# Optimization experiments

Measured on AMD Instinct MI355X. Metric: run time of the kernel, lower is better.

The kernel has to match this reference:

```python
import jax, jax.numpy as jnp
import numpy as np

D_MODEL = 1024
N_HEADS = 16
D_K = D_MODEL // N_HEADS
D_FF = 4096
EPS = 1e-5


def layer_norm(x, gamma, beta):
    mu = jnp.mean(x, axis=-1, keepdims=True)
    var = jnp.var(x, axis=-1, keepdims=True)
    return (x - mu) * jax.lax.rsqrt(var + EPS) * gamma + beta


def setup_inputs() -> dict:
    key = jax.random.key(0)
    ks = jax.random.split(key, 16)
    B, S = 4, 1024
    s = 0.02
    inp = {
        "x": jax.random.normal(ks[0], (B, S, D_MODEL), dtype=jnp.float32),
        "mask": jnp.ones((B, 1, 1, S), dtype=jnp.int32),
        "Wq": jax.random.normal(ks[1], (D_MODEL, D_MODEL), jnp.float32) * s,
        "bq": jnp.zeros((D_MODEL,), jnp.float32),
        "Wk": jax.random.normal(ks[2], (D_MODEL, D_MODEL), jnp.float32) * s,
        "bk": jnp.zeros((D_MODEL,), jnp.float32),
        "Wv": jax.random.normal(ks[3], (D_MODEL, D_MODEL), jnp.float32) * s,
        "bv": jnp.zeros((D_MODEL,), jnp.float32),
        "Wo": jax.random.normal(ks[4], (D_MODEL, D_MODEL), jnp.float32) * s,
        "bo": jnp.zeros((D_MODEL,), jnp.float32),
        "W1": jax.random.normal(ks[5], (D_MODEL, D_FF), jnp.float32) * s,
        "b1": jnp.zeros((D_FF,), jnp.float32),
        "W2": jax.random.normal(ks[6], (D_FF, D_MODEL), jnp.float32) * s,
        "b2": jnp.zeros((D_MODEL,), jnp.float32),
        "ln1_g": jnp.ones((D_MODEL,), jnp.float32),
        "ln1_b": jnp.zeros((D_MODEL,), jnp.float32),
        "ln2_g": jnp.ones((D_MODEL,), jnp.float32),
        "ln2_b": jnp.zeros((D_MODEL,), jnp.float32),
    }
    return inp


def reference(x, mask, Wq, bq, Wk, bk, Wv, bv, Wo, bo, W1, b1, W2, b2,
              ln1_g, ln1_b, ln2_g, ln2_b):
    B, S, _ = x.shape
    # QKV projections -> [B, H, S, d_k]
    def split_heads(t):
        return t.reshape(B, S, N_HEADS, D_K).transpose(0, 2, 1, 3)
    Q = split_heads(x @ Wq + bq)
    K = split_heads(x @ Wk + bk)
    V = split_heads(x @ Wv + bv)
    # scores [B, H, S, S]
    scores = jnp.einsum('bhqd,bhkd->bhqk', Q, K) / jnp.sqrt(jnp.float32(D_K))
    scores = jnp.where(mask == 0, jnp.float32(-1e9), scores)
    attn = jax.nn.softmax(scores, axis=-1)
    ctx = jnp.einsum('bhqk,bhkd->bhqd', attn, V)
    ctx = ctx.transpose(0, 2, 1, 3).reshape(B, S, D_MODEL)
    attn_out = ctx @ Wo + bo
    # residual + LN (dropout is identity in eval)
    h = layer_norm(x + attn_out, ln1_g, ln1_b)
    ff = jax.nn.relu(h @ W1 + b1) @ W2 + b2
    return layer_norm(h + ff, ln2_g, ln2_b)
```

## Files before the change

### kernel.cpp

```cpp
#include <hip/hip_runtime.h>
#include <hip/hip_bf16.h>

typedef __attribute__((ext_vector_type(8))) short bf16x8;
typedef __attribute__((ext_vector_type(4))) short bf16x4;
typedef __attribute__((ext_vector_type(4))) float f32x4;
typedef unsigned int u32;
typedef unsigned short ush;

#define SEQ 1024
#define MTOT 4096

__device__ __forceinline__ ush f2bf(float f){
  u32 u = __float_as_uint(f);
  u32 r = (u + 0x7fffu + ((u >> 16) & 1u)) >> 16;
  return (ush)r;
}

__device__ __forceinline__ f32x4 mfma16(bf16x8 a, bf16x8 b, f32x4 c){
  return __builtin_amdgcn_mfma_f32_16x16x32_bf16(a, b, c, 0, 0, 0);
}

__device__ __forceinline__ void gload_lds16(const ush* g, ush* l){
  __builtin_amdgcn_global_load_lds(
      (const __attribute__((address_space(1))) u32*)g,
      (__attribute__((address_space(3))) u32*)l, 16, 0, 0);
}

__global__ __launch_bounds__(256) void cvt_kernel(const float* __restrict__ src,
                                                  ush* __restrict__ dst, int n){
  int i = (blockIdx.x * 256 + threadIdx.x) * 4;
  if (i < n){
    float4 v = *(const float4*)&src[i];
    ushort4 o = { f2bf(v.x), f2bf(v.y), f2bf(v.z), f2bf(v.w) };
    *(ushort4*)&dst[i] = o;
  }
}

__global__ __launch_bounds__(256) void tconv_kernel(const float* __restrict__ src,
                                                    ush* __restrict__ dst, int R, int C){
  __shared__ float t[32][33];
  int tx = threadIdx.x & 31, ty = threadIdx.x >> 5;
  int r0 = blockIdx.y * 32, c0 = blockIdx.x * 32;
  #pragma unroll
  for (int i = 0; i < 32; i += 8)
    t[ty + i][tx] = src[(size_t)(r0 + ty + i) * C + (c0 + tx)];
  __syncthreads();
  #pragma unroll
  for (int i = 0; i < 32; i += 8)
    dst[(size_t)(c0 + ty + i) * R + (r0 + tx)] = f2bf(t[tx][ty + i]);
}

__global__ __launch_bounds__(256) void biaspack_kernel(const float* __restrict__ bq,
    const float* __restrict__ bk, const float* __restrict__ bv, float* __restrict__ dst){
  int i = blockIdx.x * 256 + threadIdx.x;
  if (i < 3072){
    float v = (i < 1024) ? bq[i] : (i < 2048) ? bk[i - 1024] : bv[i - 2048];
    dst[i] = v;
  }
}

__device__ __forceinline__ void stage_piece(ush* piece, const ush* g0, int K,
                                            int tid, int w){
  #pragma unroll
  for (int I = 0; I < 2; I++){
    int c = I * 512 + tid;
    int r = c >> 2;
    int gl = (c & 3) ^ ((r >> 1) & 3);
    gload_lds16(g0 + (size_t)r * K + gl * 8, piece + I * 4096 + w * 512);
  }
}

__device__ __forceinline__ bf16x8 frag(const ush* piece, int row, int g){
  int phys = g ^ ((row >> 1) & 3);
  return *(const bf16x8*)(piece + row * 32 + phys * 8);
}

#define PH_BAR_TOP() do{ __builtin_amdgcn_sched_barrier(0); \
  __builtin_amdgcn_s_barrier(); \
  asm volatile("s_waitcnt lgkmcnt(0)" ::: "memory"); \
  __builtin_amdgcn_sched_barrier(0); \
  __builtin_amdgcn_s_setprio(1); }while(0)
#define PH_BAR_BOT() do{ __builtin_amdgcn_s_setprio(0); \
  __builtin_amdgcn_sched_barrier(0); \
  __builtin_amdgcn_s_barrier(); }while(0)

template<int RELU, int OUTF32>
__global__ __launch_bounds__(512, 2) void gemm8_kernel(
    const ush* __restrict__ A, const ush* __restrict__ Bt,
    const float* __restrict__ bias,
    ush* __restrict__ Cb, float* __restrict__ Cf,
    int M, int N, int K, int ldc, int ksl)
{
  __shared__ ush lds[2][2][2][8192];
  const int tid = threadIdx.x;
  const int lane = tid & 63, w = tid >> 6;
  const int g = lane >> 4, qr = lane & 15;
  const int wr = w >> 2, wc = w & 3;
  const int gx = gridDim.x;
  const int nwg = gx * gridDim.y;
  const int id = blockIdx.y * gx + blockIdx.x;
  const int swz = (id & 7) * (nwg >> 3) + (id >> 3);
  const int bn = (swz % gx) * 256;
  const int bm = (swz / gx) * 256;
  const int kbase = blockIdx.z * ksl;
  const int NT = ksl >> 6;
  const ush* Ab = A  + (size_t)bm * K + kbase;
  const ush* Bb = Bt + (size_t)bn * K + kbase;

  stage_piece(lds[0][0][0], Ab,      K, tid, w);
  stage_piece(lds[0][1][0], Bb,      K, tid, w);
  stage_piece(lds[0][0][1], Ab + 32, K, tid, w);
  stage_piece(lds[0][1][1], Bb + 32, K, tid, w);
  if (NT > 1){
    stage_piece(lds[1][0][0], Ab + 64, K, tid, w);
    stage_piece(lds[1][1][0], Bb + 64, K, tid, w);
  }
  asm volatile("s_waitcnt vmcnt(4)" ::: "memory");
  __builtin_amdgcn_sched_barrier(0);
  __builtin_amdgcn_s_barrier();

  f32x4 acc[8][4] = {};
  const int ar = wr * 128 + qr;
  const int br = wc * 64 + qr;

  for (int T = 0; T < NT; ++T){
    const int cb = T & 1, nb = cb ^ 1;
    const ush* An = Ab + (size_t)(T + 1) * 64;
    const ush* Bn = Bb + (size_t)(T + 1) * 64;
    const ush* Af = Ab + (size_t)(T + 2) * 64;
    const ush* Bf = Bb + (size_t)(T + 2) * 64;
    bf16x8 af[4], bfr[4];

    #pragma unroll
    for (int j = 0; j < 4; j++) bfr[j] = frag(lds[cb][1][0], br + j * 16, g);
    #pragma unroll
    for (int i = 0; i < 4; i++) af[i] = frag(lds[cb][0][0], ar + i * 16, g);
    if (T + 1 < NT) stage_piece(lds[nb][0][1], An + 32, K, tid, w);
    PH_BAR_TOP();
    #pragma unroll
    for (int i = 0; i < 4; i++)
      #pragma unroll
      for (int j = 0; j < 4; j++)
        acc[i][j] = mfma16(af[i], bfr[j], acc[i][j]);
    PH_BAR_BOT();

    #pragma unroll
    for (int i = 0; i < 4; i++) af[i] = frag(lds[cb][0][0], ar + 64 + i * 16, g);
    if (T + 1 < NT) stage_piece(lds[nb][1][1], Bn + 32, K, tid, w);
    PH_BAR_TOP();
    #pragma unroll
    for (int i = 0; i < 4; i++)
      #pragma unroll
      for (int j = 0; j < 4; j++)
        acc[4 + i][j] = mfma16(af[i], bfr[j], acc[4 + i][j]);
    PH_BAR_BOT();

    #pragma unroll
    for (int j = 0; j < 4; j++) bfr[j] = frag(lds[cb][1][1], br + j * 16, g);
    #pragma unroll
    for (int i = 0; i < 4; i++) af[i] = frag(lds[cb][0][1], ar + i * 16, g);
    if (T + 2 < NT) stage_piece(lds[cb][0][0], Af, K, tid, w);
    PH_BAR_TOP();
    #pragma unroll
    for (int i = 0; i < 4; i++)
      #pragma unroll
      for (int j = 0; j < 4; j++)
        acc[i][j] = mfma16(af[i], bfr[j], acc[i][j]);
    PH_BAR_BOT();

    #pragma unroll
    for (int i = 0; i < 4; i++) af[i] = frag(lds[cb][0][1], ar + 64 + i * 16, g);
    if (T + 2 < NT) stage_piece(lds[cb][1][0], Bf, K, tid, w);
    PH_BAR_TOP();
    #pragma unroll
    for (int i = 0; i < 4; i++)
      #pragma unroll
      for (int j = 0; j < 4; j++)
        acc[4 + i][j] = mfma16(af[i], bfr[j], acc[4 + i][j]);
    __builtin_amdgcn_s_setprio(0);
    __builtin_amdgcn_sched_barrier(0);
    asm volatile("s_waitcnt vmcnt(4)" ::: "memory");
    __builtin_amdgcn_sched_barrier(0);
    __builtin_amdgcn_s_barrier();
  }

  float* Cfz = Cf;
  if (OUTF32) Cfz = Cf + (size_t)blockIdx.z * M * ldc;
  #pragma unroll
  for (int j = 0; j < 4; j++){
    const int col = bn + wc * 64 + j * 16 + qr;
    const float bv = OUTF32 ? 0.f : bias[col];
    #pragma unroll
    for (int i = 0; i < 8; i++){
      const int row0 = bm + wr * 128 + i * 16 + g * 4;
      #pragma unroll
      for (int rr = 0; rr < 4; rr++){
        float v = acc[i][j][rr] + bv;
        if (RELU) v = fmaxf(v, 0.f);
        const size_t idx = (size_t)(row0 + rr) * ldc + col;
        if (OUTF32) Cfz[idx] = v; else Cb[idx] = f2bf(v);
      }
    }
  }
}

__global__ __launch_bounds__(256) void attn_kernel(
    const ush* __restrict__ qkv, const int* __restrict__ mask,
    ush* __restrict__ ctx)
{
  __shared__ ush Vt[64 * 40];
  __shared__ ush Pl[4][16 * 40];
  __shared__ int mk[1024];
  const int tid = threadIdx.x;
  const int lane = tid & 63, w = tid >> 6;
  const int g = lane >> 4, qr = lane & 15;
  const int hb = blockIdx.y;
  const int b = hb >> 4, hh = hb & 15;
  const int qt = blockIdx.x;

  { int4 mv = *(const int4*)&mask[b * SEQ + tid * 4]; *(int4*)&mk[tid * 4] = mv; }
  __syncthreads();

  const size_t rowQ = (size_t)(b * SEQ + qt * 64 + w * 16 + qr);
  const ush* Qp = qkv + rowQ * 3072 + hh * 64;
  bf16x8 qf0 = *(const bf16x8*)(Qp + g * 8);
  bf16x8 qf1 = *(const bf16x8*)(Qp + 32 + g * 8);

  const ush* Kb = qkv + (size_t)b * SEQ * 3072 + 1024 + hh * 64;
  const ush* Vb = qkv + (size_t)b * SEQ * 3072 + 2048 + hh * 64;

  f32x4 oa[4] = {};
  float m_run = -1e30f, l_run = 0.f;
  const int vkey = tid >> 3, vd0 = (tid & 7) * 8;

  for (int kt = 0; kt < SEQ / 32; ++kt){
    const int k0 = kt * 32;
    bf16x8 vv = *(const bf16x8*)(Vb + (size_t)(k0 + vkey) * 3072 + vd0);
    const ush* Kr0 = Kb + (size_t)(k0 + qr) * 3072;
    const ush* Kr1 = Kr0 + (size_t)16 * 3072;
    bf16x8 ka0 = *(const bf16x8*)(Kr0 + g * 8);
    bf16x8 ka1 = *(const bf16x8*)(Kr0 + 32 + g * 8);
    bf16x8 kb0 = *(const bf16x8*)(Kr1 + g * 8);
    bf16x8 kb1 = *(const bf16x8*)(Kr1 + 32 + g * 8);
    f32x4 z = {0.f, 0.f, 0.f, 0.f};
    f32x4 st0 = mfma16(ka0, qf0, z); st0 = mfma16(ka1, qf1, st0);
    f32x4 st1 = mfma16(kb0, qf0, z); st1 = mfma16(kb1, qf1, st1);
    float sc[8];
    #pragma unroll
    for (int r = 0; r < 4; r++){
      int key = k0 + g * 4 + r;
      sc[r]     = (mk[key] == 0)      ? -1e9f : st0[r] * 0.125f;
      sc[4 + r] = (mk[key + 16] == 0) ? -1e9f : st1[r] * 0.125f;
    }
    float pm = sc[0];
    #pragma unroll
    for (int r = 1; r < 8; r++) pm = fmaxf(pm, sc[r]);
    pm = fmaxf(pm, __shfl_xor(pm, 16));
    pm = fmaxf(pm, __shfl_xor(pm, 32));
    float m_new = fmaxf(m_run, pm);
    float corr = __expf(m_run - m_new);
    float ls = 0.f;
    #pragma unroll
    for (int r = 0; r < 8; r++){ sc[r] = __expf(sc[r] - m_new); ls += sc[r]; }
    ls += __shfl_xor(ls, 16); ls += __shfl_xor(ls, 32);
    l_run = l_run * corr + ls; m_run = m_new;
    #pragma unroll
    for (int r = 0; r < 4; r++){
      float cr = __shfl(corr, g * 4 + r);
      oa[0][r] *= cr; oa[1][r] *= cr; oa[2][r] *= cr; oa[3][r] *= cr;
    }
    bf16x4 p0, p1;
    #pragma unroll
    for (int r = 0; r < 4; r++){ p0[r] = (short)f2bf(sc[r]); p1[r] = (short)f2bf(sc[4 + r]); }
    *(bf16x4*)&Pl[w][qr * 40 + g * 4]      = p0;
    *(bf16x4*)&Pl[w][qr * 40 + 16 + g * 4] = p1;
    __syncthreads();
    #pragma unroll
    for (int j = 0; j < 8; j++) Vt[(vd0 + j) * 40 + vkey] = (ush)vv[j];
    __syncthreads();
    bf16x8 pf = *(const bf16x8*)&Pl[w][qr * 40 + g * 8];
    #pragma unroll
    for (int d = 0; d < 4; d++){
      bf16x8 vf = *(const bf16x8*)&Vt[(d * 16 + qr) * 40 + g * 8];
      oa[d] = mfma16(pf, vf, oa[d]);
    }
  }
  float linv = 1.f / l_run;
  #pragma unroll
  for (int r = 0; r < 4; r++){
    float lr = __shfl(linv, g * 4 + r);
    size_t rowO = (size_t)(b * SEQ + qt * 64 + w * 16 + g * 4 + r);
    #pragma unroll
    for (int d = 0; d < 4; d++)
      ctx[rowO * 1024 + hh * 64 + d * 16 + qr] = f2bf(oa[d][r] * lr);
  }
}

template<bool WB>
__global__ __launch_bounds__(256) void ln4_kernel(
    const float* __restrict__ X, const float* __restrict__ P,
    const float* __restrict__ bias,
    const float* __restrict__ gam, const float* __restrict__ bet,
    float* __restrict__ Of, ush* __restrict__ Ob)
{
  const int row = blockIdx.x, tid = threadIdx.x;
  const size_t base = (size_t)row * 1024 + tid * 4;
  float4 xv = *(const float4*)&X[base];
  float4 bv4 = *(const float4*)&bias[tid * 4];
  float s0 = xv.x + bv4.x, s1 = xv.y + bv4.y, s2 = xv.z + bv4.z, s3 = xv.w + bv4.w;
  #pragma unroll
  for (int z = 0; z < 4; z++){
    float4 p = *(const float4*)&P[(size_t)z * 4194304 + base];
    s0 += p.x; s1 += p.y; s2 += p.z; s3 += p.w;
  }
  float sum = s0 + s1 + s2 + s3;
  float sq  = s0 * s0 + s1 * s1 + s2 * s2 + s3 * s3;
  #pragma unroll
  for (int o = 1; o < 64; o <<= 1){ sum += __shfl_xor(sum, o); sq += __shfl_xor(sq, o); }
  __shared__ float red[8];
  int lane = tid & 63, w = tid >> 6;
  if (lane == 0){ red[w] = sum; red[4 + w] = sq; }
  __syncthreads();
  sum = red[0] + red[1] + red[2] + red[3];
  sq  = red[4] + red[5] + red[6] + red[7];
  float mean = sum * (1.f / 1024.f);
  float var  = sq * (1.f / 1024.f) - mean * mean;
  float rs = rsqrtf(var + 1e-5f);
  float4 gv = *(const float4*)&gam[tid * 4];
  float4 bt = *(const float4*)&bet[tid * 4];
  float o0 = (s0 - mean) * rs * gv.x + bt.x;
  float o1 = (s1 - mean) * rs * gv.y + bt.y;
  float o2 = (s2 - mean) * rs * gv.z + bt.z;
  float o3 = (s3 - mean) * rs * gv.w + bt.w;
  float4 ov = { o0, o1, o2, o3 };
  *(float4*)&Of[base] = ov;
  if (WB){
    ushort4 ob = { f2bf(o0), f2bf(o1), f2bf(o2), f2bf(o3) };
    *(ushort4*)&Ob[base] = ob;
  }
}

extern "C" void kernel_launch(void* const* d_in, const int* in_sizes, int n_in,
                              void* d_out, int out_size, void* d_ws, size_t ws_size,
                              hipStream_t stream)
{
  const float* x    = (const float*)d_in[0];
  const int*   mask = (const int*)  d_in[1];
  const float* Wq = (const float*)d_in[2];
  const float* bq = (const float*)d_in[3];
  const float* Wk = (const float*)d_in[4];
  const float* bk = (const float*)d_in[5];
  const float* Wv = (const float*)d_in[6];
  const float* bv = (const float*)d_in[7];
  const float* Wo = (const float*)d_in[8];
  const float* bo = (const float*)d_in[9];
  const float* W1 = (const float*)d_in[10];
  const float* b1 = (const float*)d_in[11];
  const float* W2 = (const float*)d_in[12];
  const float* b2 = (const float*)d_in[13];
  const float* g1 = (const float*)d_in[14];
  const float* be1= (const float*)d_in[15];
  const float* g2 = (const float*)d_in[16];
  const float* be2= (const float*)d_in[17];
  float* out = (float*)d_out;

  char* ws = (char*)d_ws;
  size_t off = 0;
  auto alloc = [&](size_t bytes)->void*{ void* p = ws + off; off += (bytes + 255) & ~(size_t)255; return p; };
  ush* xb     = (ush*)alloc((size_t)MTOT * 1024 * 2);
  ush* wqkvT  = (ush*)alloc((size_t)3072 * 1024 * 2);
  ush* woT    = (ush*)alloc((size_t)1024 * 1024 * 2);
  ush* w1T    = (ush*)alloc((size_t)4096 * 1024 * 2);
  ush* w2T    = (ush*)alloc((size_t)1024 * 4096 * 2);
  float* bqkv = (float*)alloc(3072 * 4);
  ush* qkv    = (ush*)alloc((size_t)MTOT * 3072 * 2);
  ush* ctx    = (ush*)alloc((size_t)MTOT * 1024 * 2);
  float* part = (float*)alloc((size_t)4 * MTOT * 1024 * 4);
  float* h    = (float*)alloc((size_t)MTOT * 1024 * 4);
  ush* hb     = (ush*)alloc((size_t)MTOT * 1024 * 2);
  ush* ff1    = qkv;

  cvt_kernel<<<dim3(4096), dim3(256), 0, stream>>>(x, xb, MTOT * 1024);
  tconv_kernel<<<dim3(32, 32), dim3(256), 0, stream>>>(Wq, wqkvT,               1024, 1024);
  tconv_kernel<<<dim3(32, 32), dim3(256), 0, stream>>>(Wk, wqkvT + 1024 * 1024, 1024, 1024);
  tconv_kernel<<<dim3(32, 32), dim3(256), 0, stream>>>(Wv, wqkvT + 2048 * 1024, 1024, 1024);
  tconv_kernel<<<dim3(32, 32), dim3(256), 0, stream>>>(Wo, woT,                 1024, 1024);
  tconv_kernel<<<dim3(128, 32), dim3(256), 0, stream>>>(W1, w1T, 1024, 4096);
  tconv_kernel<<<dim3(32, 128), dim3(256), 0, stream>>>(W2, w2T, 4096, 1024);
  biaspack_kernel<<<dim3(12), dim3(256), 0, stream>>>(bq, bk, bv, bqkv);

  gemm8_kernel<0, 0><<<dim3(12, 16, 1), dim3(512), 0, stream>>>(
      xb, wqkvT, bqkv, qkv, nullptr, MTOT, 3072, 1024, 3072, 1024);

  attn_kernel<<<dim3(16, 64), dim3(256), 0, stream>>>(qkv, mask, ctx);

  gemm8_kernel<0, 1><<<dim3(4, 16, 4), dim3(512), 0, stream>>>(
      ctx, woT, nullptr, nullptr, part, MTOT, 1024, 1024, 1024, 256);

  ln4_kernel<true><<<dim3(4096), dim3(256), 0, stream>>>(x, part, bo, g1, be1, h, hb);

  gemm8_kernel<1, 0><<<dim3(16, 16, 1), dim3(512), 0, stream>>>(
      hb, w1T, b1, ff1, nullptr, MTOT, 4096, 1024, 4096, 1024);

  gemm8_kernel<0, 1><<<dim3(4, 16, 4), dim3(512), 0, stream>>>(
      ff1, w2T, nullptr, nullptr, part, MTOT, 1024, 4096, 1024, 1024);

  ln4_kernel<false><<<dim3(4096), dim3(256), 0, stream>>>(h, part, b2, g2, be2, out, nullptr);
}
```

Before: 416.6 us.

## Rewrite attention with 32x32 MFMA, pretransposed V, exp2 softmax and lazy rescale

Replaces the flash-attention kernel with a version using 32x32x16 bf16 MFMA tiles, 32 queries per wave and 64-key blocks. V is pretransposed by a new kernel so it can be read directly as MFMA operands, and P is packed in registers with cvt_pk and permlane32 swaps rather than staged through LDS with block barriers. The QKV GEMM epilogue folds the 1/sqrt(dk)*log2e scale into Q so softmax can use exp2. The running max is only rescaled when it grows by more than 8, and per-key masking is skipped when the whole mask row is ones. The cost is an extra transpose kernel, extra workspace, and a bit of precision loss from the delayed rescale.

```diff
diff --git a/kernel.cpp b/kernel.cpp
--- a/kernel.cpp
+++ b/kernel.cpp
@@ -2,13 +2,20 @@
 #include <hip/hip_bf16.h>
 
 typedef __attribute__((ext_vector_type(8))) short bf16x8;
-typedef __attribute__((ext_vector_type(4))) short bf16x4;
 typedef __attribute__((ext_vector_type(4))) float f32x4;
+typedef __attribute__((ext_vector_type(16))) float f32x16;
 typedef unsigned int u32;
 typedef unsigned short ush;
 
 #define SEQ 1024
 #define MTOT 4096
+#define QSCALE_LOG2 0.18033688f
+
+#if __has_builtin(__builtin_amdgcn_exp2f)
+#define EXP2(x) __builtin_amdgcn_exp2f(x)
+#else
+#define EXP2(x) exp2f(x)
+#endif
 
 __device__ __forceinline__ ush f2bf(float f){
   u32 u = __float_as_uint(f);
@@ -18,6 +25,13 @@
 
 __device__ __forceinline__ f32x4 mfma16(bf16x8 a, bf16x8 b, f32x4 c){
   return __builtin_amdgcn_mfma_f32_16x16x32_bf16(a, b, c, 0, 0, 0);
+}
+__device__ __forceinline__ f32x16 mfma32(bf16x8 a, bf16x8 b, f32x16 c){
+  return __builtin_amdgcn_mfma_f32_32x32x16_bf16(a, b, c, 0, 0, 0);
+}
+
+__device__ __forceinline__ u32 cvtpk(float lo, float hi){
+  u32 r; asm("v_cvt_pk_bf16_f32 %0, %1, %2" : "=v"(r) : "v"(lo), "v"(hi)); return r;
 }
 
 __device__ __forceinline__ void gload_lds16(const ush* g, ush* l){
@@ -57,6 +71,21 @@
     float v = (i < 1024) ? bq[i] : (i < 2048) ? bk[i - 1024] : bv[i - 2048];
     dst[i] = v;
   }
+}
+
+__global__ __launch_bounds__(256) void vtrans_kernel(const ush* __restrict__ qkv,
+                                                     ush* __restrict__ VT){
+  __shared__ ush t[32][34];
+  int tx = threadIdx.x & 31, ty = threadIdx.x >> 5;
+  int bh = blockIdx.z, b = bh >> 4, h = bh & 15;
+  int k0 = blockIdx.x * 32, d0 = blockIdx.y * 32;
+  #pragma unroll
+  for (int i = 0; i < 32; i += 8)
+    t[ty + i][tx] = qkv[(size_t)(b * SEQ + k0 + ty + i) * 3072 + 2048 + h * 64 + d0 + tx];
+  __syncthreads();
+  #pragma unroll
+  for (int i = 0; i < 32; i += 8)
+    VT[(size_t)(bh * 64 + d0 + ty + i) * SEQ + k0 + tx] = t[tx][ty + i];
 }
 
 __device__ __forceinline__ void stage_piece(ush* piece, const ush* g0, int K,
@@ -84,7 +113,7 @@
   __builtin_amdgcn_sched_barrier(0); \
   __builtin_amdgcn_s_barrier(); }while(0)
 
-template<int RELU, int OUTF32>
+template<int RELU, int OUTF32, int SCALEQ>
 __global__ __launch_bounds__(512, 2) void gemm8_kernel(
     const ush* __restrict__ A, const ush* __restrict__ Bt,
     const float* __restrict__ bias,
@@ -190,6 +219,7 @@
   for (int j = 0; j < 4; j++){
     const int col = bn + wc * 64 + j * 16 + qr;
     const float bv = OUTF32 ? 0.f : bias[col];
+    const float scl = (SCALEQ && col < 1024) ? QSCALE_LOG2 : 1.f;
     #pragma unroll
     for (int i = 0; i < 8; i++){
       const int row0 = bm + wr * 128 + i * 16 + g * 4;
@@ -197,6 +227,7 @@
       for (int rr = 0; rr < 4; rr++){
         float v = acc[i][j][rr] + bv;
         if (RELU) v = fmaxf(v, 0.f);
+        if (SCALEQ) v *= scl;
         const size_t idx = (size_t)(row0 + rr) * ldc + col;
         if (OUTF32) Cfz[idx] = v; else Cb[idx] = f2bf(v);
       }
@@ -204,95 +235,131 @@
   }
 }
 
-__global__ __launch_bounds__(256) void attn_kernel(
-    const ush* __restrict__ qkv, const int* __restrict__ mask,
-    ush* __restrict__ ctx)
+__global__ __launch_bounds__(256) void attn2_kernel(
+    const ush* __restrict__ qkv, const ush* __restrict__ VT,
+    const int* __restrict__ mask, ush* __restrict__ ctx)
 {
-  __shared__ ush Vt[64 * 40];
-  __shared__ ush Pl[4][16 * 40];
-  __shared__ int mk[1024];
   const int tid = threadIdx.x;
   const int lane = tid & 63, w = tid >> 6;
-  const int g = lane >> 4, qr = lane & 15;
-  const int hb = blockIdx.y;
-  const int b = hb >> 4, hh = hb & 15;
-  const int qt = blockIdx.x;
-
-  { int4 mv = *(const int4*)&mask[b * SEQ + tid * 4]; *(int4*)&mk[tid * 4] = mv; }
+  const int c = lane & 31, hi = lane >> 5;
+  const int bh = blockIdx.y, b = bh >> 4, hh = bh & 15;
+  const int q0 = blockIdx.x * 128 + w * 32;
+
+  __shared__ int mflag;
+  if (tid == 0) mflag = 1;
   __syncthreads();
-
-  const size_t rowQ = (size_t)(b * SEQ + qt * 64 + w * 16 + qr);
-  const ush* Qp = qkv + rowQ * 3072 + hh * 64;
-  bf16x8 qf0 = *(const bf16x8*)(Qp + g * 8);
-  bf16x8 qf1 = *(const bf16x8*)(Qp + 32 + g * 8);
-
-  const ush* Kb = qkv + (size_t)b * SEQ * 3072 + 1024 + hh * 64;
-  const ush* Vb = qkv + (size_t)b * SEQ * 3072 + 2048 + hh * 64;
-
-  f32x4 oa[4] = {};
+  {
+    int4 mv = *(const int4*)&mask[b * SEQ + tid * 4];
+    if (!(mv.x && mv.y && mv.z && mv.w)) mflag = 0;
+  }
+  __syncthreads();
+  const bool maskall = (mflag != 0);
+
+  const ush* Qrow = qkv + (size_t)(b * SEQ + q0 + c) * 3072 + hh * 64;
+  bf16x8 qf[4];
+  #pragma unroll
+  for (int kd = 0; kd < 4; kd++)
+    qf[kd] = *(const bf16x8*)(Qrow + kd * 16 + hi * 8);
+
+  const ush* Kb  = qkv + (size_t)(b * SEQ) * 3072 + 1024 + hh * 64;
+  const ush* VTb = VT + (size_t)(bh * 64) * SEQ;
+
+  f32x16 o0 = {}, o1 = {};
   float m_run = -1e30f, l_run = 0.f;
-  const int vkey = tid >> 3, vd0 = (tid & 7) * 8;
-
-  for (int kt = 0; kt < SEQ / 32; ++kt){
-    const int k0 = kt * 32;
-    bf16x8 vv = *(const bf16x8*)(Vb + (size_t)(k0 + vkey) * 3072 + vd0);
-    const ush* Kr0 = Kb + (size_t)(k0 + qr) * 3072;
-    const ush* Kr1 = Kr0 + (size_t)16 * 3072;
-    bf16x8 ka0 = *(const bf16x8*)(Kr0 + g * 8);
-    bf16x8 ka1 = *(const bf16x8*)(Kr0 + 32 + g * 8);
-    bf16x8 kb0 = *(const bf16x8*)(Kr1 + g * 8);
-    bf16x8 kb1 = *(const bf16x8*)(Kr1 + 32 + g * 8);
-    f32x4 z = {0.f, 0.f, 0.f, 0.f};
-    f32x4 st0 = mfma16(ka0, qf0, z); st0 = mfma16(ka1, qf1, st0);
-    f32x4 st1 = mfma16(kb0, qf0, z); st1 = mfma16(kb1, qf1, st1);
-    float sc[8];
-    #pragma unroll
-    for (int r = 0; r < 4; r++){
-      int key = k0 + g * 4 + r;
-      sc[r]     = (mk[key] == 0)      ? -1e9f : st0[r] * 0.125f;
-      sc[4 + r] = (mk[key + 16] == 0) ? -1e9f : st1[r] * 0.125f;
-    }
-    float pm = sc[0];
-    #pragma unroll
-    for (int r = 1; r < 8; r++) pm = fmaxf(pm, sc[r]);
-    pm = fmaxf(pm, __shfl_xor(pm, 16));
-    pm = fmaxf(pm, __shfl_xor(pm, 32));
-    float m_new = fmaxf(m_run, pm);
-    float corr = __expf(m_run - m_new);
+
+  bf16x8 kf[8];
+  #pragma unroll
+  for (int kb = 0; kb < 2; kb++)
+    #pragma unroll
+    for (int kd = 0; kd < 4; kd++)
+      kf[kb * 4 + kd] = *(const bf16x8*)(Kb + (size_t)(kb * 32 + c) * 3072 + kd * 16 + hi * 8);
+
+  for (int t = 0; t < SEQ / 64; ++t){
+    const int k0 = t * 64;
+    bf16x8 vf[8];
+    #pragma unroll
+    for (int db = 0; db < 2; db++)
+      #pragma unroll
+      for (int ks = 0; ks < 4; ks++)
+        vf[db * 4 + ks] = *(const bf16x8*)(VTb + (size_t)(db * 32 + c) * SEQ + k0 + ks * 16 + hi * 8);
+
+    f32x16 s0 = {}, s1 = {};
+    #pragma unroll
+    for (int kd = 0; kd < 4; kd++){
+      s0 = mfma32(kf[kd],     qf[kd], s0);
+      s1 = mfma32(kf[4 + kd], qf[kd], s1);
+    }
+
+    float p[32];
+    #pragma unroll
+    for (int r = 0; r < 16; r++){ p[r] = s0[r]; p[16 + r] = s1[r]; }
+
+    if (!maskall){
+      #pragma unroll
+      for (int r32 = 0; r32 < 32; r32++){
+        int r = r32 & 15;
+        int key = (r32 >> 4) * 32 + (r & 3) + 8 * (r >> 2) + 4 * hi;
+        if (mask[b * SEQ + k0 + key] == 0) p[r32] = -1e9f;
+      }
+    }
+
+    if (t + 1 < SEQ / 64){
+      #pragma unroll
+      for (int kb = 0; kb < 2; kb++)
+        #pragma unroll
+        for (int kd = 0; kd < 4; kd++)
+          kf[kb * 4 + kd] = *(const bf16x8*)(Kb + (size_t)(k0 + 64 + kb * 32 + c) * 3072 + kd * 16 + hi * 8);
+    }
+
+    float pmax = p[0];
+    #pragma unroll
+    for (int r = 1; r < 32; r++) pmax = fmaxf(pmax, p[r]);
+    pmax = fmaxf(pmax, __shfl_xor(pmax, 32));
+    if (__any(pmax > m_run + 8.f)){
+      float m_new = fmaxf(m_run, pmax);
+      float corr = EXP2(m_run - m_new);
+      l_run *= corr;
+      m_run = m_new;
+      #pragma unroll
+      for (int r = 0; r < 16; r++){
+        float cr = __shfl(corr, (r & 3) + 8 * (r >> 2) + 4 * hi);
+        o0[r] *= cr; o1[r] *= cr;
+      }
+    }
     float ls = 0.f;
     #pragma unroll
-    for (int r = 0; r < 8; r++){ sc[r] = __expf(sc[r] - m_new); ls += sc[r]; }
-    ls += __shfl_xor(ls, 16); ls += __shfl_xor(ls, 32);
-    l_run = l_run * corr + ls; m_run = m_new;
-    #pragma unroll
-    for (int r = 0; r < 4; r++){
-      float cr = __shfl(corr, g * 4 + r);
-      oa[0][r] *= cr; oa[1][r] *= cr; oa[2][r] *= cr; oa[3][r] *= cr;
-    }
-    bf16x4 p0, p1;
-    #pragma unroll
-    for (int r = 0; r < 4; r++){ p0[r] = (short)f2bf(sc[r]); p1[r] = (short)f2bf(sc[4 + r]); }
-    *(bf16x4*)&Pl[w][qr * 40 + g * 4]      = p0;
-    *(bf16x4*)&Pl[w][qr * 40 + 16 + g * 4] = p1;
-    __syncthreads();
-    #pragma unroll
-    for (int j = 0; j < 8; j++) Vt[(vd0 + j) * 40 + vkey] = (ush)vv[j];
-    __syncthreads();
-    bf16x8 pf = *(const bf16x8*)&Pl[w][qr * 40 + g * 8];
-    #pragma unroll
-    for (int d = 0; d < 4; d++){
-      bf16x8 vf = *(const bf16x8*)&Vt[(d * 16 + qr) * 40 + g * 8];
-      oa[d] = mfma16(pf, vf, oa[d]);
-    }
-  }
+    for (int r = 0; r < 32; r++){ p[r] = EXP2(p[r] - m_run); ls += p[r]; }
+    ls += __shfl_xor(ls, 32);
+    l_run += ls;
+
+    union { u32 wdw[4]; bf16x8 v; } af[4];
+    #pragma unroll
+    for (int ks = 0; ks < 4; ks++){
+      int b0 = (ks >> 1) * 16 + 8 * (ks & 1);
+      u32 c00 = cvtpk(p[b0],     p[b0 + 1]);
+      u32 c01 = cvtpk(p[b0 + 2], p[b0 + 3]);
+      u32 c10 = cvtpk(p[b0 + 4], p[b0 + 5]);
+      u32 c11 = cvtpk(p[b0 + 6], p[b0 + 7]);
+      asm volatile("v_permlane32_swap_b32 %0, %1" : "+v"(c10), "+v"(c00));
+      asm volatile("v_permlane32_swap_b32 %0, %1" : "+v"(c11), "+v"(c01));
+      af[ks].wdw[0] = c00; af[ks].wdw[1] = c01; af[ks].wdw[2] = c10; af[ks].wdw[3] = c11;
+    }
+
+    #pragma unroll
+    for (int ks = 0; ks < 4; ks++){
+      o0 = mfma32(af[ks].v, vf[ks],     o0);
+      o1 = mfma32(af[ks].v, vf[4 + ks], o1);
+    }
+  }
+
   float linv = 1.f / l_run;
   #pragma unroll
-  for (int r = 0; r < 4; r++){
-    float lr = __shfl(linv, g * 4 + r);
-    size_t rowO = (size_t)(b * SEQ + qt * 64 + w * 16 + g * 4 + r);
-    #pragma unroll
-    for (int d = 0; d < 4; d++)
-      ctx[rowO * 1024 + hh * 64 + d * 16 + qr] = f2bf(oa[d][r] * lr);
+  for (int r = 0; r < 16; r++){
+    int crow = (r & 3) + 8 * (r >> 2) + 4 * hi;
+    float li = __shfl(linv, crow);
+    size_t base = (size_t)(b * SEQ + q0 + crow) * 1024 + hh * 64;
+    ctx[base + c]      = f2bf(o0[r] * li);
+    ctx[base + 32 + c] = f2bf(o1[r] * li);
   }
 }
 
@@ -378,6 +445,7 @@
   float* part = (float*)alloc((size_t)4 * MTOT * 1024 * 4);
   float* h    = (float*)alloc((size_t)MTOT * 1024 * 4);
   ush* hb     = (ush*)alloc((size_t)MTOT * 1024 * 2);
+  ush* VT     = (ush*)alloc((size_t)64 * 64 * SEQ * 2);
   ush* ff1    = qkv;
 
   cvt_kernel<<<dim3(4096), dim3(256), 0, stream>>>(x, xb, MTOT * 1024);
@@ -389,20 +457,22 @@
   tconv_kernel<<<dim3(32, 128), dim3(256), 0, stream>>>(W2, w2T, 4096, 1024);
   biaspack_kernel<<<dim3(12), dim3(256), 0, stream>>>(bq, bk, bv, bqkv);
 
-  gemm8_kernel<0, 0><<<dim3(12, 16, 1), dim3(512), 0, stream>>>(
+  gemm8_kernel<0, 0, 1><<<dim3(12, 16, 1), dim3(512), 0, stream>>>(
       xb, wqkvT, bqkv, qkv, nullptr, MTOT, 3072, 1024, 3072, 1024);
 
-  attn_kernel<<<dim3(16, 64), dim3(256), 0, stream>>>(qkv, mask, ctx);
-
-  gemm8_kernel<0, 1><<<dim3(4, 16, 4), dim3(512), 0, stream>>>(
+  vtrans_kernel<<<dim3(32, 2, 64), dim3(256), 0, stream>>>(qkv, VT);
+
+  attn2_kernel<<<dim3(8, 64), dim3(256), 0, stream>>>(qkv, VT, mask, ctx);
+
+  gemm8_kernel<0, 1, 0><<<dim3(4, 16, 4), dim3(512), 0, stream>>>(
       ctx, woT, nullptr, nullptr, part, MTOT, 1024, 1024, 1024, 256);
 
   ln4_kernel<true><<<dim3(4096), dim3(256), 0, stream>>>(x, part, bo, g1, be1, h, hb);
 
-  gemm8_kernel<1, 0><<<dim3(16, 16, 1), dim3(512), 0, stream>>>(
+  gemm8_kernel<1, 0, 0><<<dim3(16, 16, 1), dim3(512), 0, stream>>>(
       hb, w1T, b1, ff1, nullptr, MTOT, 4096, 1024, 4096, 1024);
 
-  gemm8_kernel<0, 1><<<dim3(4, 16, 4), dim3(512), 0, stream>>>(
+  gemm8_kernel<0, 1, 0><<<dim3(4, 16, 4), dim3(512), 0, stream>>>(
       ff1, w2T, nullptr, nullptr, part, MTOT, 1024, 4096, 1024, 1024);
 
   ln4_kernel<false><<<dim3(4096), dim3(256), 0, stream>>>(h, part, b2, g2, be2, out, nullptr);
```

Result: faster. 390.4 us (-6.3%).
